# Kernel optimization log

Hardware: AMD Instinct MI355X
Metric: run time of the kernel (lower is better)

Reference implementation:

```python
import jax, jax.numpy as jnp
import numpy as np

N_NODES = 200000
N_EDGES = 6400000
N_REL = 16


def rgcn_layer(x, src, dst, etype, W, root, b, num_nodes):
    # FastRGCNConv math: per-edge m_e = x[src_e] @ W[etype_e], mean-aggregated at dst,
    # plus root transform and bias. We precompute x @ W for all relations (N,R,Fout)
    # then gather per edge -- avoids materializing per-edge (Fin,Fout) weight copies.
    xW = jnp.einsum('nf,rfo->nro', x, W)          # [N, R, Fout]
    msg = xW[src, etype]                           # [E, Fout] gather
    agg = jax.ops.segment_sum(msg, dst, num_segments=num_nodes)
    deg = jax.ops.segment_sum(jnp.ones((src.shape[0],), x.dtype), dst,
                              num_segments=num_nodes)
    agg = agg / jnp.maximum(deg, 1.0)[:, None]     # mean aggregation (0 for isolated nodes)
    return agg + x @ root + b


def setup_inputs() -> dict:
    key = jax.random.key(0)
    ks = jax.random.split(key, 8)
    x = jax.random.normal(ks[0], (N_NODES, 7), dtype=jnp.float32)
    edge_index = jax.random.randint(ks[1], (2, N_EDGES), 0, N_NODES, dtype=jnp.int64)
    edge_type = jax.random.randint(ks[2], (N_EDGES,), 0, N_REL, dtype=jnp.int64)
    W1 = jax.random.normal(ks[3], (N_REL, 7, 16), dtype=jnp.float32) * 0.3
    root1 = jax.random.normal(ks[4], (7, 16), dtype=jnp.float32) * 0.3
    b1 = jnp.zeros((16,), dtype=jnp.float32)
    W2 = jax.random.normal(ks[5], (N_REL, 16, 2), dtype=jnp.float32) * 0.3
    root2 = jax.random.normal(ks[6], (16, 2), dtype=jnp.float32) * 0.3
    b2 = jnp.zeros((2,), dtype=jnp.float32)
    return {"x": x, "edge_index": edge_index, "edge_type": edge_type,
            "W1": W1, "root1": root1, "b1": b1,
            "W2": W2, "root2": root2, "b2": b2}


def reference(x, edge_index, edge_type, W1, root1, b1, W2, root2, b2):
    num_nodes = x.shape[0]
    src, dst = edge_index[0], edge_index[1]
    h = jax.nn.relu(rgcn_layer(x, src, dst, edge_type, W1, root1, b1, num_nodes))
    out = rgcn_layer(h, src, dst, edge_type, W2, root2, b2, num_nodes)
    return jax.nn.log_softmax(out, axis=1)
```

## Files before the change

### kernel.cpp

```cpp
#include <hip/hip_runtime.h>
#include <hip/hip_fp16.h>
#include <math.h>


#define BLOCK 256
#define NREL 16
#define DBIN 256
#define BKT_ST 17
#define CH   8192
#define BINS_MAX   1024
#define CHUNKS_MAX 1024
#define SCAN 1024

#define SC2  1048576.0f
#define ISC2 (1.0f/1048576.0f)
#define HQS  16.0f
#define IHQS (1.0f/16.0f)


__device__ __forceinline__ long long q8f(float v) {
    v = fminf(fmaxf(v, -14.f), 14.f);
    return (long long)(int)rintf(v * 8.0f);
}

__device__ __forceinline__ unsigned long long pack7x(const float* xp) {
    long long t = q8f(xp[0]) + (q8f(xp[1]) << 8) + (q8f(xp[2]) << 16)
                + (q8f(xp[3]) << 24) + (q8f(xp[4]) << 32) + (q8f(xp[5]) << 40)
                + (q8f(xp[6]) << 48) + (1LL << 56);
    return (unsigned long long)t;
}

__device__ __forceinline__ void unpack7x(long long t, float* f, float* cnt) {
#pragma unroll
    for (int i = 0; i < 7; ++i) {
        int fi = (int)(signed char)(t & 0xFF);
        t = (t - fi) >> 8;
        f[i] = fi * 0.125f;
    }
    *cnt = (float)(int)t;
}

__device__ __forceinline__ float2 uh2f2(unsigned u) {
    __half2 t; __builtin_memcpy(&t, &u, 4);
    return __half22float2(t);
}
__device__ __forceinline__ unsigned f2uh2(float a, float b) {
    __half2 t = __floats2half2_rn(a, b);
    unsigned u; __builtin_memcpy(&u, &t, 4);
    return u;
}


__global__ __launch_bounds__(BLOCK) void k_prep(
    const float* __restrict__ x, unsigned long long* __restrict__ qx, int N)
{
    int n = blockIdx.x * BLOCK + threadIdx.x;
    if (n < N) qx[n] = pack7x(x + (size_t)n * 7);
}


__global__ __launch_bounds__(BLOCK) void k_hist(
    const int* __restrict__ dst, unsigned* __restrict__ chunkCnt,
    unsigned* __restrict__ binTotal, int E, int nb)
{
    __shared__ unsigned hist[BINS_MAX];
    for (int i = threadIdx.x; i < nb; i += BLOCK) hist[i] = 0;
    __syncthreads();
    int base = blockIdx.x * CH;
#pragma unroll 4
    for (int k = 0; k < CH / BLOCK; ++k) {
        int e = base + k * BLOCK + threadIdx.x;
        if (e < E) atomicAdd(&hist[(unsigned)dst[e] >> 8], 1u);
    }
    __syncthreads();
    for (int i = threadIdx.x; i < nb; i += BLOCK) {
        unsigned c = hist[i];
        chunkCnt[(size_t)blockIdx.x * nb + i] = c;
        if (c) atomicAdd(&binTotal[i], c);
    }
}

__global__ __launch_bounds__(BLOCK) void k_scan(
    const unsigned* __restrict__ chunkCnt, const unsigned* __restrict__ binTotal,
    unsigned* __restrict__ chunkOfs, unsigned* __restrict__ binBase,
    int nb, int nc)
{
    __shared__ unsigned sA[SCAN], sB[SCAN];
    int b = blockIdx.x;

    unsigned* cur = sA; unsigned* nxt = sB;
    for (int i = threadIdx.x; i < SCAN; i += BLOCK)
        cur[i] = (i < nb) ? binTotal[i] : 0u;
    __syncthreads();
    for (int ofs = 1; ofs < SCAN; ofs <<= 1) {
        for (int i = threadIdx.x; i < SCAN; i += BLOCK)
            nxt[i] = cur[i] + ((i >= ofs) ? cur[i - ofs] : 0u);
        __syncthreads();
        unsigned* t = cur; cur = nxt; nxt = t;
    }
    unsigned binBase_b = (b > 0) ? cur[b - 1] : 0u;
    if (threadIdx.x == 0) binBase[b] = binBase_b;
    __syncthreads();

    for (int i = threadIdx.x; i < SCAN; i += BLOCK)
        cur[i] = (i < nc) ? chunkCnt[(size_t)i * nb + b] : 0u;
    __syncthreads();
    for (int ofs = 1; ofs < SCAN; ofs <<= 1) {
        for (int i = threadIdx.x; i < SCAN; i += BLOCK)
            nxt[i] = cur[i] + ((i >= ofs) ? cur[i - ofs] : 0u);
        __syncthreads();
        unsigned* t = cur; cur = nxt; nxt = t;
    }
    for (int i = threadIdx.x; i < nc; i += BLOCK)
        chunkOfs[(size_t)i * nb + b] = binBase_b + ((i > 0) ? cur[i - 1] : 0u);
}

__global__ __launch_bounds__(BLOCK) void k_scatter2(
    const int* __restrict__ src, const int* __restrict__ dst,
    const int* __restrict__ et, const unsigned* __restrict__ chunkCnt,
    const unsigned* __restrict__ chunkOfs, unsigned* __restrict__ rec,
    int E, int nb)
{
    __shared__ unsigned stg[CH];
    __shared__ unsigned lofs[BINS_MAX];
    __shared__ unsigned curi[BINS_MAX];
    __shared__ unsigned gofs[BINS_MAX];

    int c = blockIdx.x;

    unsigned* sA = stg;
    unsigned* sB = stg + SCAN;
    for (int i = threadIdx.x; i < SCAN; i += BLOCK)
        sA[i] = (i < nb) ? chunkCnt[(size_t)c * nb + i] : 0u;
    __syncthreads();
    unsigned* curp = sA; unsigned* nxtp = sB;
    for (int ofs = 1; ofs < SCAN; ofs <<= 1) {
        for (int i = threadIdx.x; i < SCAN; i += BLOCK)
            nxtp[i] = curp[i] + ((i >= ofs) ? curp[i - ofs] : 0u);
        __syncthreads();
        unsigned* t = curp; curp = nxtp; nxtp = t;
    }
    for (int i = threadIdx.x; i < nb; i += BLOCK) {
        unsigned l = (i > 0) ? curp[i - 1] : 0u;
        lofs[i] = l;
        curi[i] = l;
        gofs[i] = chunkOfs[(size_t)c * nb + i];
    }
    __syncthreads();

    int base = c * CH;
#pragma unroll 4
    for (int k = 0; k < CH / BLOCK; ++k) {
        int e = base + k * BLOCK + threadIdx.x;
        if (e < E) {
            unsigned d = (unsigned)dst[e];
            unsigned bin = d >> 8;
            unsigned slot = atomicAdd(&curi[bin], 1u);
            stg[slot] = (unsigned)src[e] | ((unsigned)et[e] << 18) | ((d & 255u) << 22);
        }
    }
    __syncthreads();

    for (int b = threadIdx.x; b < nb; b += BLOCK) {
        unsigned s0 = lofs[b], s1 = curi[b], g = gofs[b];
        for (unsigned i = s0; i < s1; ++i) rec[g + (i - s0)] = stg[i];
    }
}


__global__ __launch_bounds__(BLOCK) void k_agg1(
    const float* __restrict__ x, const unsigned long long* __restrict__ qx,
    const unsigned* __restrict__ rec,
    const unsigned* __restrict__ binBase, const unsigned* __restrict__ binTotal,
    const float* __restrict__ W1, const float* __restrict__ root1,
    const float* __restrict__ b1, unsigned* __restrict__ h2,
    uint4* __restrict__ qh, float* __restrict__ deg, int N)
{
    __shared__ unsigned long long bkt[DBIN * BKT_ST];
    __shared__ float w[NREL * 112];
    __shared__ float r1[112];
    __shared__ float bb[16];

    for (int i = threadIdx.x; i < DBIN * BKT_ST; i += BLOCK) bkt[i] = 0ull;
    for (int i = threadIdx.x; i < NREL * 112; i += BLOCK) w[i] = W1[i];
    if (threadIdx.x < 112) r1[threadIdx.x] = root1[threadIdx.x];
    if (threadIdx.x < 16) bb[threadIdx.x] = b1[threadIdx.x];
    __syncthreads();

    int b = blockIdx.x;
    unsigned base = binBase[b], cnt = binTotal[b];
    for (unsigned i = threadIdx.x; i < cnt; i += BLOCK) {
        unsigned rc = rec[base + i];
        int s  = rc & 0x3FFFF;
        int r  = (rc >> 18) & 15;
        int dl = (rc >> 22) & 255;
        atomicAdd(&bkt[dl * BKT_ST + r], qx[s]);
    }
    __syncthreads();

    int dl = threadIdx.x;
    int n = b * DBIN + dl;
    if (n >= N) return;

    float acc[16];
#pragma unroll
    for (int o = 0; o < 16; ++o) acc[o] = 0.f;
    float dg = 0.f;
#pragma unroll
    for (int r = 0; r < NREL; ++r) {
        float sv[7], c;
        unpack7x((long long)bkt[dl * BKT_ST + r], sv, &c);
        dg += c;
#pragma unroll
        for (int f = 0; f < 7; ++f) {
            float xf = sv[f];
#pragma unroll
            for (int o = 0; o < 16; ++o) acc[o] += xf * w[r * 112 + f * 16 + o];
        }
    }

    float invd = 1.0f / fmaxf(dg, 1.0f);
    float xv[7];
    const float* xp = x + (size_t)n * 7;
#pragma unroll
    for (int f = 0; f < 7; ++f) xv[f] = xp[f];

    float hv[16];
#pragma unroll
    for (int oo = 0; oo < 16; ++oo) {
        float v = bb[oo] + acc[oo] * invd;
#pragma unroll
        for (int f = 0; f < 7; ++f) v += xv[f] * r1[f * 16 + oo];
        hv[oo] = fmaxf(v, 0.f);
    }
    uint4* hp = (uint4*)(h2 + ((size_t)n << 3));
    hp[0] = make_uint4(f2uh2(hv[0], hv[1]),  f2uh2(hv[2], hv[3]),
                       f2uh2(hv[4], hv[5]),  f2uh2(hv[6], hv[7]));
    hp[1] = make_uint4(f2uh2(hv[8], hv[9]),  f2uh2(hv[10], hv[11]),
                       f2uh2(hv[12], hv[13]), f2uh2(hv[14], hv[15]));

    unsigned p[4];
#pragma unroll
    for (int g = 0; g < 4; ++g) {
        unsigned v = 0;
#pragma unroll
        for (int j = 0; j < 4; ++j) {
            unsigned q = (unsigned)(int)rintf(fminf(hv[g * 4 + j], 15.9f) * HQS);
            v |= q << (8 * j);
        }
        p[g] = v;
    }
    qh[n] = make_uint4(p[0], p[1], p[2], p[3]);
    deg[n] = dg;
}

__global__ __launch_bounds__(BLOCK) void k_agg2(
    const unsigned* __restrict__ h2, const uint4* __restrict__ qh,
    const unsigned* __restrict__ rec,
    const unsigned* __restrict__ binBase, const unsigned* __restrict__ binTotal,
    const float* __restrict__ deg, const float* __restrict__ W2,
    const float* __restrict__ root2, const float* __restrict__ b2,
    float* __restrict__ out, int N)
{
    __shared__ unsigned long long a2q[DBIN];
    __shared__ float w[NREL * 32];
    __shared__ float r2[32];
    __shared__ float bb[2];

    for (int i = threadIdx.x; i < DBIN; i += BLOCK) a2q[i] = 0ull;
    for (int i = threadIdx.x; i < NREL * 32; i += BLOCK) w[i] = W2[i];
    if (threadIdx.x < 32) r2[threadIdx.x] = root2[threadIdx.x];
    if (threadIdx.x < 2) bb[threadIdx.x] = b2[threadIdx.x];
    __syncthreads();

    int b = blockIdx.x;
    unsigned base = binBase[b], cnt = binTotal[b];
    for (unsigned i = threadIdx.x; i < cnt; i += BLOCK) {
        unsigned rc = rec[base + i];
        int s  = rc & 0x3FFFF;
        int r  = (rc >> 18) & 15;
        int dl = (rc >> 22) & 255;

        uint4 q = qh[s];
        const float* wr = &w[r * 32];
        float a0 = 0.f, a1 = 0.f;
        unsigned qs[4] = {q.x, q.y, q.z, q.w};
#pragma unroll
        for (int g = 0; g < 4; ++g) {
            unsigned v = qs[g];
#pragma unroll
            for (int j = 0; j < 4; ++j) {
                float f = (float)((v >> (8 * j)) & 0xFFu) * IHQS;
                int ff = g * 4 + j;
                a0 += f * wr[ff * 2 + 0];
                a1 += f * wr[ff * 2 + 1];
            }
        }
        long long p0 = (long long)(int)rintf(a0 * SC2);
        long long p1 = (long long)(int)rintf(a1 * SC2);
        atomicAdd(&a2q[dl], (unsigned long long)(p0 + (p1 << 32)));
    }
    __syncthreads();

    int dl = threadIdx.x;
    int n = b * DBIN + dl;
    if (n >= N) return;

    float invd = 1.0f / fmaxf(deg[n], 1.0f);
    float o0 = bb[0], o1 = bb[1];
    const uint4* hp = (const uint4*)(h2 + ((size_t)n << 3));
    uint4 qa = hp[0], qb = hp[1];
    unsigned qs[8] = {qa.x, qa.y, qa.z, qa.w, qb.x, qb.y, qb.z, qb.w};
#pragma unroll
    for (int p = 0; p < 8; ++p) {
        float2 f = uh2f2(qs[p]);
        o0 += f.x * r2[(p * 2 + 0) * 2 + 0] + f.y * r2[(p * 2 + 1) * 2 + 0];
        o1 += f.x * r2[(p * 2 + 0) * 2 + 1] + f.y * r2[(p * 2 + 1) * 2 + 1];
    }
    long long t = (long long)a2q[dl];
    int q0 = (int)(t & 0xFFFFFFFFLL);
    long long t1 = (t - (long long)q0) >> 32;
    int q1 = (int)t1;
    o0 += (q0 * ISC2) * invd;
    o1 += (q1 * ISC2) * invd;

    float m = fmaxf(o0, o1);
    float lse = m + logf(expf(o0 - m) + expf(o1 - m));
    ((float2*)out)[n] = make_float2(o0 - lse, o1 - lse);
}


__global__ __launch_bounds__(BLOCK) void k_edge1e(
    const float* __restrict__ x, const int* __restrict__ src,
    const int* __restrict__ dst, const int* __restrict__ et,
    unsigned long long* __restrict__ Sq, int E)
{
    int e = blockIdx.x * BLOCK + threadIdx.x;
    if (e >= E) return;
    int s = src[e], d = dst[e], r = et[e];
    atomicAdd(Sq + (size_t)d * NREL + r, pack7x(x + (size_t)s * 7));
}

__global__ __launch_bounds__(BLOCK) void k_node1e(
    const float* __restrict__ x, const unsigned long long* __restrict__ Sq,
    const float* __restrict__ W1, const float* __restrict__ root1,
    const float* __restrict__ b1, float* __restrict__ h,
    float* __restrict__ deg, int N)
{
    __shared__ float w[NREL * 112];
    __shared__ float r1[112];
    __shared__ float bb[16];
    for (int i = threadIdx.x; i < NREL * 112; i += BLOCK) w[i] = W1[i];
    if (threadIdx.x < 112) r1[threadIdx.x] = root1[threadIdx.x];
    if (threadIdx.x < 16) bb[threadIdx.x] = b1[threadIdx.x];
    __syncthreads();

    int n = blockIdx.x * BLOCK + threadIdx.x;
    if (n >= N) return;

    float acc[16];
#pragma unroll
    for (int o = 0; o < 16; ++o) acc[o] = 0.f;
    float dg = 0.f;

    const ulonglong2* sp = (const ulonglong2*)(Sq + ((size_t)n << 4));
#pragma unroll
    for (int rp = 0; rp < NREL / 2; ++rp) {
        ulonglong2 q = sp[rp];
#pragma unroll
        for (int half = 0; half < 2; ++half) {
            int r = rp * 2 + half;
            float sv[7], c;
            unpack7x((long long)(half ? q.y : q.x), sv, &c);
            dg += c;
#pragma unroll
            for (int f = 0; f < 7; ++f) {
                float xf = sv[f];
#pragma unroll
                for (int o = 0; o < 16; ++o) acc[o] += xf * w[r * 112 + f * 16 + o];
            }
        }
    }

    float invd = 1.0f / fmaxf(dg, 1.0f);
    float xv[7];
    const float* xp = x + (size_t)n * 7;
#pragma unroll
    for (int f = 0; f < 7; ++f) xv[f] = xp[f];

    float4* hp = (float4*)(h + ((size_t)n << 4));
#pragma unroll
    for (int og = 0; og < 4; ++og) {
        float o[4];
#pragma unroll
        for (int oi = 0; oi < 4; ++oi) {
            int oo = og * 4 + oi;
            float v = bb[oo] + acc[oo] * invd;
#pragma unroll
            for (int f = 0; f < 7; ++f) v += xv[f] * r1[f * 16 + oo];
            o[oi] = fmaxf(v, 0.f);
        }
        hp[og] = make_float4(o[0], o[1], o[2], o[3]);
    }
    deg[n] = dg;
}

__global__ __launch_bounds__(BLOCK) void k_edge2d(
    const float* __restrict__ h, const int* __restrict__ src,
    const int* __restrict__ dst, const int* __restrict__ et,
    const float* __restrict__ W2, unsigned long long* __restrict__ agg2, int E)
{
    __shared__ float w[NREL * 32];
    for (int i = threadIdx.x; i < NREL * 32; i += BLOCK) w[i] = W2[i];
    __syncthreads();

    int e = blockIdx.x * BLOCK + threadIdx.x;
    if (e >= E) return;
    int s = src[e], d = dst[e], r = et[e];

    const float4* hp = (const float4*)(h + ((size_t)s << 4));
    const float* wr = &w[r * 32];
    float a0 = 0.f, a1 = 0.f;
#pragma unroll
    for (int fg = 0; fg < 4; ++fg) {
        float4 hv = hp[fg];
        a0 += hv.x * wr[(fg * 4 + 0) * 2] + hv.y * wr[(fg * 4 + 1) * 2] +
              hv.z * wr[(fg * 4 + 2) * 2] + hv.w * wr[(fg * 4 + 3) * 2];
        a1 += hv.x * wr[(fg * 4 + 0) * 2 + 1] + hv.y * wr[(fg * 4 + 1) * 2 + 1] +
              hv.z * wr[(fg * 4 + 2) * 2 + 1] + hv.w * wr[(fg * 4 + 3) * 2 + 1];
    }
    long long p0 = (long long)(int)rintf(a0 * SC2);
    long long p1 = (long long)(int)rintf(a1 * SC2);
    atomicAdd(agg2 + d, (unsigned long long)(p0 + (p1 << 32)));
}

__global__ __launch_bounds__(BLOCK) void k_outd(
    const float* __restrict__ h, const unsigned long long* __restrict__ agg2,
    const float* __restrict__ deg, const float* __restrict__ root2,
    const float* __restrict__ b2, float* __restrict__ out, int N)
{
    __shared__ float r2[32];
    __shared__ float bb[2];
    if (threadIdx.x < 32) r2[threadIdx.x] = root2[threadIdx.x];
    if (threadIdx.x < 2) bb[threadIdx.x] = b2[threadIdx.x];
    __syncthreads();

    int n = blockIdx.x * BLOCK + threadIdx.x;
    if (n >= N) return;

    float invd = 1.0f / fmaxf(deg[n], 1.0f);
    float o0 = bb[0], o1 = bb[1];
    const float4* hp = (const float4*)(h + ((size_t)n << 4));
#pragma unroll
    for (int fg = 0; fg < 4; ++fg) {
        float4 hv = hp[fg];
        o0 += hv.x * r2[(fg * 4 + 0) * 2 + 0] + hv.y * r2[(fg * 4 + 1) * 2 + 0] +
              hv.z * r2[(fg * 4 + 2) * 2 + 0] + hv.w * r2[(fg * 4 + 3) * 2 + 0];
        o1 += hv.x * r2[(fg * 4 + 0) * 2 + 1] + hv.y * r2[(fg * 4 + 1) * 2 + 1] +
              hv.z * r2[(fg * 4 + 2) * 2 + 1] + hv.w * r2[(fg * 4 + 3) * 2 + 1];
    }
    long long t = (long long)agg2[n];
    int q0 = (int)(t & 0xFFFFFFFFLL);
    long long t1 = (t - (long long)q0) >> 32;
    int q1 = (int)t1;
    o0 += (q0 * ISC2) * invd;
    o1 += (q1 * ISC2) * invd;

    float m = fmaxf(o0, o1);
    float lse = m + logf(expf(o0 - m) + expf(o1 - m));
    ((float2*)out)[n] = make_float2(o0 - lse, o1 - lse);
}


extern "C" void kernel_launch(void* const* d_in, const int* in_sizes, int n_in,
                              void* d_out, int out_size, void* d_ws, size_t ws_size,
                              hipStream_t stream)
{
    const float* x     = (const float*)d_in[0];
    const int*   ei    = (const int*)d_in[1];
    const int*   et    = (const int*)d_in[2];
    const float* W1    = (const float*)d_in[3];
    const float* root1 = (const float*)d_in[4];
    const float* b1    = (const float*)d_in[5];
    const float* W2    = (const float*)d_in[6];
    const float* root2 = (const float*)d_in[7];
    const float* b2    = (const float*)d_in[8];
    float* out = (float*)d_out;

    const int N = in_sizes[0] / 7;
    const int E = in_sizes[1] / 2;
    const int* src = ei;
    const int* dst = ei + E;

    const int nb = (N + DBIN - 1) / DBIN;
    const int nc = (E + CH - 1) / CH;

    if (nb <= BINS_MAX && nc <= CHUNKS_MAX && N <= (1 << 18)) {
        char* base = (char*)d_ws;
        size_t ofs = 0;
        unsigned* rec      = (unsigned*)(base + ofs); ofs += (size_t)E * 4;
        ofs = (ofs + 255) & ~(size_t)255;
        unsigned long long* qx = (unsigned long long*)(base + ofs); ofs += (size_t)N * 8;
        ofs = (ofs + 255) & ~(size_t)255;
        unsigned* chunkCnt = (unsigned*)(base + ofs); ofs += (size_t)nc * nb * 4;
        ofs = (ofs + 255) & ~(size_t)255;
        unsigned* chunkOfs = (unsigned*)(base + ofs); ofs += (size_t)nc * nb * 4;
        ofs = (ofs + 255) & ~(size_t)255;
        unsigned* binTotal = (unsigned*)(base + ofs); ofs += (size_t)nb * 4;
        ofs = (ofs + 255) & ~(size_t)255;
        unsigned* binBase  = (unsigned*)(base + ofs); ofs += (size_t)nb * 4;
        ofs = (ofs + 255) & ~(size_t)255;
        unsigned* h2 = (unsigned*)(base + ofs); ofs += (size_t)N * 32;
        ofs = (ofs + 255) & ~(size_t)255;
        uint4* qh = (uint4*)(base + ofs); ofs += (size_t)N * 16;
        float* deg = (float*)(base + ofs); ofs += (size_t)N * 4;

        hipMemsetAsync(binTotal, 0, (size_t)nb * 4, stream);

        int npb = (N + BLOCK - 1) / BLOCK;
        k_prep    <<<npb, BLOCK, 0, stream>>>(x, qx, N);
        k_hist    <<<nc, BLOCK, 0, stream>>>(dst, chunkCnt, binTotal, E, nb);
        k_scan    <<<nb, BLOCK, 0, stream>>>(chunkCnt, binTotal, chunkOfs, binBase, nb, nc);
        k_scatter2<<<nc, BLOCK, 0, stream>>>(src, dst, et, chunkCnt, chunkOfs, rec, E, nb);
        k_agg1    <<<nb, BLOCK, 0, stream>>>(x, qx, rec, binBase, binTotal, W1, root1, b1, h2, qh, deg, N);
        k_agg2    <<<nb, BLOCK, 0, stream>>>(h2, qh, rec, binBase, binTotal, deg, W2, root2, b2, out, N);
    } else {
        int eb = (E + BLOCK - 1) / BLOCK;
        int nbk = (N + BLOCK - 1) / BLOCK;
        char* wbase = (char*)d_ws;
        size_t agg2_ofs = (size_t)N * 128;
        size_t h_ofs    = (agg2_ofs + (size_t)N * 8 + 255) & ~(size_t)255;
        size_t deg_ofs  = h_ofs + (size_t)N * 64;

        unsigned long long* Sq   = (unsigned long long*)wbase;
        unsigned long long* agg2 = (unsigned long long*)(wbase + agg2_ofs);
        float*              h    = (float*)(wbase + h_ofs);
        float*              deg  = (float*)(wbase + deg_ofs);

        hipMemsetAsync(Sq, 0, agg2_ofs + (size_t)N * 8, stream);
        k_edge1e<<<eb, BLOCK, 0, stream>>>(x, src, dst, et, Sq, E);
        k_node1e<<<nbk, BLOCK, 0, stream>>>(x, Sq, W1, root1, b1, h, deg, N);
        k_edge2d<<<eb, BLOCK, 0, stream>>>(h, src, dst, et, W2, agg2, E);
        k_outd<<<nbk, BLOCK, 0, stream>>>(h, agg2, deg, root2, b2, out, N);
    }
}
```

Before: 373.3 us.

## Move per-chunk bin scan into histogram kernel and coalesce scatter writeout

The histogram kernel now loads dst as int4 vectors and also computes each chunk's exclusive prefix of bin counts with a wave-shuffle scan, storing it to a new global array. The scatter kernel reads that array instead of redoing a 10-step shared-memory scan, loads src/dst/etype as int4, and writes the staged records out with one thread per element, finding each element's bin by binary search. Before, one thread copied each bin serially. This is meant to remove redundant scan work and uncoalesced per-bin copy loops. In exchange it adds an extra workspace array and a binary search per element, and the fast path now requires E to be divisible by 4.

```diff
diff --git a/kernel.cpp b/kernel.cpp
--- a/kernel.cpp
+++ b/kernel.cpp
@@ -61,23 +61,71 @@
 
 __global__ __launch_bounds__(BLOCK) void k_hist(
     const int* __restrict__ dst, unsigned* __restrict__ chunkCnt,
-    unsigned* __restrict__ binTotal, int E, int nb)
+    unsigned* __restrict__ binTotal, unsigned* __restrict__ lofsG,
+    int E, int nb)
 {
     __shared__ unsigned hist[BINS_MAX];
+    __shared__ unsigned wsum[BLOCK / 64];
     for (int i = threadIdx.x; i < nb; i += BLOCK) hist[i] = 0;
     __syncthreads();
-    int base = blockIdx.x * CH;
-#pragma unroll 4
-    for (int k = 0; k < CH / BLOCK; ++k) {
-        int e = base + k * BLOCK + threadIdx.x;
-        if (e < E) atomicAdd(&hist[(unsigned)dst[e] >> 8], 1u);
-    }
-    __syncthreads();
+
+    int c = blockIdx.x;
+    int base = c * CH;
+    const int4* dst4 = (const int4*)(dst + base);
+#pragma unroll
+    for (int k = 0; k < CH / (BLOCK * 4); ++k) {
+        int item = k * BLOCK + threadIdx.x;
+        int e0 = base + item * 4;
+        if (e0 + 3 < E) {
+            int4 d = dst4[item];
+            atomicAdd(&hist[(unsigned)d.x >> 8], 1u);
+            atomicAdd(&hist[(unsigned)d.y >> 8], 1u);
+            atomicAdd(&hist[(unsigned)d.z >> 8], 1u);
+            atomicAdd(&hist[(unsigned)d.w >> 8], 1u);
+        } else {
+#pragma unroll
+            for (int j = 0; j < 4; ++j) {
+                int e = e0 + j;
+                if (e < E) atomicAdd(&hist[(unsigned)dst[e] >> 8], 1u);
+            }
+        }
+    }
+    __syncthreads();
+
     for (int i = threadIdx.x; i < nb; i += BLOCK) {
-        unsigned c = hist[i];
-        chunkCnt[(size_t)blockIdx.x * nb + i] = c;
-        if (c) atomicAdd(&binTotal[i], c);
-    }
+        unsigned cn = hist[i];
+        chunkCnt[(size_t)c * nb + i] = cn;
+        if (cn) atomicAdd(&binTotal[i], cn);
+    }
+
+    unsigned v[4];
+    unsigned tsum = 0;
+#pragma unroll
+    for (int j = 0; j < 4; ++j) {
+        int bi = 4 * (int)threadIdx.x + j;
+        v[j] = (bi < nb) ? hist[bi] : 0u;
+        tsum += v[j];
+    }
+    int lane = threadIdx.x & 63, wid = threadIdx.x >> 6;
+    unsigned inc = tsum;
+#pragma unroll
+    for (int ofs = 1; ofs < 64; ofs <<= 1) {
+        unsigned o = (unsigned)__shfl_up((int)inc, ofs);
+        if (lane >= ofs) inc += o;
+    }
+    if (lane == 63) wsum[wid] = inc;
+    __syncthreads();
+    unsigned wofs = 0;
+    for (int w = 0; w < wid; ++w) wofs += wsum[w];
+    unsigned run = wofs + inc - tsum;
+    unsigned* lg = lofsG + (size_t)c * (nb + 1);
+#pragma unroll
+    for (int j = 0; j < 4; ++j) {
+        int bi = 4 * (int)threadIdx.x + j;
+        if (bi < nb) lg[bi] = run;
+        run += v[j];
+    }
+    if ((int)threadIdx.x == BLOCK - 1) lg[nb] = run;
 }
 
 __global__ __launch_bounds__(BLOCK) void k_scan(
@@ -115,55 +163,74 @@
         chunkOfs[(size_t)i * nb + b] = binBase_b + ((i > 0) ? cur[i - 1] : 0u);
 }
 
-__global__ __launch_bounds__(BLOCK) void k_scatter2(
+__global__ __launch_bounds__(BLOCK) void k_scatter3(
     const int* __restrict__ src, const int* __restrict__ dst,
-    const int* __restrict__ et, const unsigned* __restrict__ chunkCnt,
+    const int* __restrict__ et, const unsigned* __restrict__ lofsG,
     const unsigned* __restrict__ chunkOfs, unsigned* __restrict__ rec,
     int E, int nb)
 {
     __shared__ unsigned stg[CH];
-    __shared__ unsigned lofs[BINS_MAX];
+    __shared__ unsigned short lofs[BINS_MAX + 1];
     __shared__ unsigned curi[BINS_MAX];
-    __shared__ unsigned gofs[BINS_MAX];
 
     int c = blockIdx.x;
-
-    unsigned* sA = stg;
-    unsigned* sB = stg + SCAN;
-    for (int i = threadIdx.x; i < SCAN; i += BLOCK)
-        sA[i] = (i < nb) ? chunkCnt[(size_t)c * nb + i] : 0u;
-    __syncthreads();
-    unsigned* curp = sA; unsigned* nxtp = sB;
-    for (int ofs = 1; ofs < SCAN; ofs <<= 1) {
-        for (int i = threadIdx.x; i < SCAN; i += BLOCK)
-            nxtp[i] = curp[i] + ((i >= ofs) ? curp[i - ofs] : 0u);
-        __syncthreads();
-        unsigned* t = curp; curp = nxtp; nxtp = t;
-    }
-    for (int i = threadIdx.x; i < nb; i += BLOCK) {
-        unsigned l = (i > 0) ? curp[i - 1] : 0u;
-        lofs[i] = l;
-        curi[i] = l;
-        gofs[i] = chunkOfs[(size_t)c * nb + i];
+    const unsigned* lg = lofsG + (size_t)c * (nb + 1);
+    for (int i = threadIdx.x; i <= nb; i += BLOCK) {
+        unsigned l = lg[i];
+        lofs[i] = (unsigned short)l;
+        if (i < nb) curi[i] = l;
     }
     __syncthreads();
 
     int base = c * CH;
-#pragma unroll 4
-    for (int k = 0; k < CH / BLOCK; ++k) {
-        int e = base + k * BLOCK + threadIdx.x;
-        if (e < E) {
-            unsigned d = (unsigned)dst[e];
-            unsigned bin = d >> 8;
-            unsigned slot = atomicAdd(&curi[bin], 1u);
-            stg[slot] = (unsigned)src[e] | ((unsigned)et[e] << 18) | ((d & 255u) << 22);
-        }
-    }
-    __syncthreads();
-
-    for (int b = threadIdx.x; b < nb; b += BLOCK) {
-        unsigned s0 = lofs[b], s1 = curi[b], g = gofs[b];
-        for (unsigned i = s0; i < s1; ++i) rec[g + (i - s0)] = stg[i];
+    const int4* src4 = (const int4*)(src + base);
+    const int4* dst4 = (const int4*)(dst + base);
+    const int4* et4  = (const int4*)(et + base);
+#pragma unroll
+    for (int k = 0; k < CH / (BLOCK * 4); ++k) {
+        int item = k * BLOCK + threadIdx.x;
+        int e0 = base + item * 4;
+        if (e0 + 3 < E) {
+            int4 s = src4[item], d = dst4[item], t = et4[item];
+            {
+                unsigned slot = atomicAdd(&curi[(unsigned)d.x >> 8], 1u);
+                stg[slot] = (unsigned)s.x | ((unsigned)t.x << 18) | (((unsigned)d.x & 255u) << 22);
+            }
+            {
+                unsigned slot = atomicAdd(&curi[(unsigned)d.y >> 8], 1u);
+                stg[slot] = (unsigned)s.y | ((unsigned)t.y << 18) | (((unsigned)d.y & 255u) << 22);
+            }
+            {
+                unsigned slot = atomicAdd(&curi[(unsigned)d.z >> 8], 1u);
+                stg[slot] = (unsigned)s.z | ((unsigned)t.z << 18) | (((unsigned)d.z & 255u) << 22);
+            }
+            {
+                unsigned slot = atomicAdd(&curi[(unsigned)d.w >> 8], 1u);
+                stg[slot] = (unsigned)s.w | ((unsigned)t.w << 18) | (((unsigned)d.w & 255u) << 22);
+            }
+        } else {
+#pragma unroll
+            for (int j = 0; j < 4; ++j) {
+                int e = e0 + j;
+                if (e < E) {
+                    unsigned d = (unsigned)dst[e];
+                    unsigned slot = atomicAdd(&curi[d >> 8], 1u);
+                    stg[slot] = (unsigned)src[e] | ((unsigned)et[e] << 18) | ((d & 255u) << 22);
+                }
+            }
+        }
+    }
+    __syncthreads();
+
+    int total = min(CH, E - base);
+    const unsigned* cofs = chunkOfs + (size_t)c * nb;
+    for (int i = threadIdx.x; i < total; i += BLOCK) {
+        int lo = 0, hi = nb;
+        while (hi - lo > 1) {
+            int mid = (lo + hi) >> 1;
+            if ((int)lofs[mid] <= i) lo = mid; else hi = mid;
+        }
+        rec[cofs[lo] + (unsigned)(i - (int)lofs[lo])] = stg[i];
     }
 }
 
@@ -495,7 +562,7 @@
     const int nb = (N + DBIN - 1) / DBIN;
     const int nc = (E + CH - 1) / CH;
 
-    if (nb <= BINS_MAX && nc <= CHUNKS_MAX && N <= (1 << 18)) {
+    if (nb <= BINS_MAX && nc <= CHUNKS_MAX && N <= (1 << 18) && (E % 4) == 0) {
         char* base = (char*)d_ws;
         size_t ofs = 0;
         unsigned* rec      = (unsigned*)(base + ofs); ofs += (size_t)E * 4;
@@ -506,6 +573,8 @@
         ofs = (ofs + 255) & ~(size_t)255;
         unsigned* chunkOfs = (unsigned*)(base + ofs); ofs += (size_t)nc * nb * 4;
         ofs = (ofs + 255) & ~(size_t)255;
+        unsigned* lofsG    = (unsigned*)(base + ofs); ofs += (size_t)nc * (nb + 1) * 4;
+        ofs = (ofs + 255) & ~(size_t)255;
         unsigned* binTotal = (unsigned*)(base + ofs); ofs += (size_t)nb * 4;
         ofs = (ofs + 255) & ~(size_t)255;
         unsigned* binBase  = (unsigned*)(base + ofs); ofs += (size_t)nb * 4;
@@ -519,9 +588,9 @@
 
         int npb = (N + BLOCK - 1) / BLOCK;
         k_prep    <<<npb, BLOCK, 0, stream>>>(x, qx, N);
-        k_hist    <<<nc, BLOCK, 0, stream>>>(dst, chunkCnt, binTotal, E, nb);
+        k_hist    <<<nc, BLOCK, 0, stream>>>(dst, chunkCnt, binTotal, lofsG, E, nb);
         k_scan    <<<nb, BLOCK, 0, stream>>>(chunkCnt, binTotal, chunkOfs, binBase, nb, nc);
-        k_scatter2<<<nc, BLOCK, 0, stream>>>(src, dst, et, chunkCnt, chunkOfs, rec, E, nb);
+        k_scatter3<<<nc, BLOCK, 0, stream>>>(src, dst, et, lofsG, chunkOfs, rec, E, nb);
         k_agg1    <<<nb, BLOCK, 0, stream>>>(x, qx, rec, binBase, binTotal, W1, root1, b1, h2, qh, deg, N);
         k_agg2    <<<nb, BLOCK, 0, stream>>>(h2, qh, rec, binBase, binTotal, deg, W2, root2, b2, out, N);
     } else {
```

Measured after the change: 325.8 us. 1.15x faster.
